# Kernel optimization log

Measured on AMD Instinct MI355X. Metric: run time of the kernel, lower is better.

Reference implementation:

```python
import jax, jax.numpy as jnp
import numpy as np

# GlobalAttention block from GATESynergy: to_dense_batch -> multi-head
# masked self-attention per graph -> scatter back to sparse + residual.
B, NMAX, DIN, DOUT, H = 512, 160, 128, 128, 4
DH = DOUT // H  # 32
COUNTS = np.where(np.arange(B) % 2 == 0, 96, 160)  # nodes per graph, sum=65536
T = int(COUNTS.sum())


def _xavier(key, dout, din):
    lim = np.sqrt(6.0 / (din + dout)).astype(np.float32)
    return jax.random.uniform(key, (dout, din), jnp.float32, -lim, lim)


def setup_inputs() -> dict:
    key = jax.random.key(0)
    ks = jax.random.split(key, 5)
    batch = jnp.asarray(np.repeat(np.arange(B), COUNTS), dtype=jnp.int32)
    x = jax.random.normal(ks[0], (T, DIN), jnp.float32)
    return {
        "x": x,
        "batch": batch,
        "Wq": _xavier(ks[1], DOUT, DIN), "bq": jnp.zeros((DOUT,), jnp.float32),
        "Wk": _xavier(ks[2], DOUT, DIN), "bk": jnp.zeros((DOUT,), jnp.float32),
        "Wv": _xavier(ks[3], DOUT, DIN), "bv": jnp.zeros((DOUT,), jnp.float32),
        "Wo": _xavier(ks[4], DOUT, DOUT), "bo": jnp.zeros((DOUT,), jnp.float32),
    }


def reference(x, batch, Wq, bq, Wk, bk, Wv, bv, Wo, bo):
    n = x.shape[0]
    # --- to_dense_batch: sparse [T, D] -> dense [B, NMAX, D] + mask ---
    counts = jax.ops.segment_sum(jnp.ones(n, jnp.int32), batch, num_segments=B)
    starts = jnp.cumsum(counts) - counts            # first node index per graph
    pos = jnp.arange(n, dtype=jnp.int32) - starts[batch]  # slot within graph
    x_dense = jnp.zeros((B, NMAX, DIN), x.dtype).at[batch, pos].set(x)
    mask = jnp.zeros((B, NMAX), bool).at[batch, pos].set(True)

    def proj(W, b):  # [B,N,DIN] -> [B,H,N,DH]
        return (x_dense @ W.T + b).reshape(B, NMAX, H, DH).transpose(0, 2, 1, 3)

    q, k, v = proj(Wq, bq), proj(Wk, bk), proj(Wv, bv)
    scores = jnp.einsum('bhnd,bhmd->bhnm', q, k) / jnp.sqrt(jnp.asarray(DH, x.dtype))
    scores = jnp.where(mask[:, None, None, :], scores, -jnp.inf)  # mask keys
    attn = jax.nn.softmax(scores, axis=-1)  # dropout p=0.0 -> identity
    out = jnp.einsum('bhnm,bhmd->bnhd', attn, v).reshape(B, NMAX, DOUT)
    out = out @ Wo.T + bo
    out_sparse = out[batch, pos]  # gather valid nodes back to sparse layout
    return out_sparse + x  # residual: in_channels == out_channels
```

## Files before the change

### kernel.cpp

```cpp
#include <hip/hip_runtime.h>

typedef unsigned short u16;
typedef unsigned int u32;
typedef __attribute__((ext_vector_type(8))) short bf16x8;
typedef __attribute__((ext_vector_type(4))) float f32x4;

__device__ __forceinline__ u16 f2bf(float f) {
  u32 u = __builtin_bit_cast(u32, f);
  u += 0x7fffu + ((u >> 16) & 1u);
  return (u16)(u >> 16);
}
__device__ __forceinline__ short f2bs(float f) { return (short)f2bf(f); }

__device__ __forceinline__ bf16x8 cvt8(const float* p) {
  f32x4 a = *reinterpret_cast<const f32x4*>(p);
  f32x4 b = *reinterpret_cast<const f32x4*>(p + 4);
  bf16x8 r;
  r[0] = f2bs(a[0]); r[1] = f2bs(a[1]); r[2] = f2bs(a[2]); r[3] = f2bs(a[3]);
  r[4] = f2bs(b[0]); r[5] = f2bs(b[1]); r[6] = f2bs(b[2]); r[7] = f2bs(b[3]);
  return r;
}
__device__ __forceinline__ bf16x8 lds8(const u16* p) {
  return *reinterpret_cast<const bf16x8*>(p);
}

#define MFMA(a, b, c) __builtin_amdgcn_mfma_f32_16x16x32_bf16((a), (b), (c), 0, 0, 0)

constexpr int DIN = 128, DOUT = 128, DH = 32;
constexpr int T = 65536;
constexpr size_t WFOFF = 0;
constexpr size_t QOFF = 65536;
constexpr size_t KOFF = QOFF + (size_t)4 * T * DH;
constexpr size_t VOFF = KOFF + (size_t)4 * T * DH;
constexpr size_t WS_NEED = (VOFF + (size_t)4 * T * DH) * 2;

__device__ __forceinline__ size_t fragoff(int mat, int ft, int ks) {
  return ((size_t)((mat * 8 + ft) * 4 + ks)) << 9;
}

__global__ void cvtw_kernel(const float* __restrict__ Wq, const float* __restrict__ Wk,
                            const float* __restrict__ Wv, const float* __restrict__ Wo,
                            u16* __restrict__ wf) {
  const int fl = blockIdx.x * 256 + threadIdx.x;
  const int lane = fl & 63, ks = (fl >> 6) & 3, ft = (fl >> 8) & 7, mat = fl >> 11;
  const float* src = mat == 0 ? Wq : mat == 1 ? Wk : mat == 2 ? Wv : Wo;
  const int lr = lane & 15, lg = lane >> 4;
  bf16x8 r = cvt8(src + (ft * 16 + lr) * DIN + ks * 32 + lg * 8);
  *reinterpret_cast<bf16x8*>(wf + (size_t)fl * 8) = r;
}

__global__ __launch_bounds__(256, 2) void qkv_kernel(const float* __restrict__ x,
                                                     const float* __restrict__ bq,
                                                     const float* __restrict__ bk,
                                                     const float* __restrict__ bv,
                                                     u16* __restrict__ ws) {
  const int tid = threadIdx.x;
  const int w = tid >> 6, lane = tid & 63, lg = lane >> 4, lr = lane & 15;
  const size_t rbase = (size_t)blockIdx.x * 128 + w * 32;
  const f32x4 zero = {0.f, 0.f, 0.f, 0.f};
  const u16* wf = ws + WFOFF;
  u16* Q = ws + QOFF;
  u16* K = ws + KOFF;
  u16* V = ws + VOFF;

  bf16x8 xa[2][4];
#pragma unroll
  for (int rt = 0; rt < 2; ++rt)
#pragma unroll
    for (int ks = 0; ks < 4; ++ks)
      xa[rt][ks] = cvt8(x + (rbase + rt * 16 + lr) * DIN + ks * 32 + lg * 8);

#pragma unroll
  for (int ft = 0; ft < 8; ++ft) {
    const int h = ft >> 1, dt = ft & 1;
    bf16x8 wqf[4], wkf[4], wvf[4];
#pragma unroll
    for (int ks = 0; ks < 4; ++ks) {
      wqf[ks] = lds8(wf + fragoff(0, ft, ks) + lane * 8);
      wkf[ks] = lds8(wf + fragoff(1, ft, ks) + lane * 8);
      wvf[ks] = lds8(wf + fragoff(2, ft, ks) + lane * 8);
    }
    f32x4 qacc[2], kacc[2], vacc[2];
#pragma unroll
    for (int rt = 0; rt < 2; ++rt) qacc[rt] = kacc[rt] = vacc[rt] = zero;
#pragma unroll
    for (int rt = 0; rt < 2; ++rt)
#pragma unroll
      for (int ks = 0; ks < 4; ++ks) {
        qacc[rt] = MFMA(xa[rt][ks], wqf[ks], qacc[rt]);
        kacc[rt] = MFMA(xa[rt][ks], wkf[ks], kacc[rt]);
        vacc[rt] = MFMA(wvf[ks], xa[rt][ks], vacc[rt]);
      }
    const float bqv = bq[ft * 16 + lr], bkv = bk[ft * 16 + lr];
    float bvj[4];
#pragma unroll
    for (int j = 0; j < 4; ++j) bvj[j] = bv[ft * 16 + lg * 4 + j];
#pragma unroll
    for (int rt = 0; rt < 2; ++rt) {
      const size_t row0 = rbase + rt * 16;
      const size_t qk_base = (size_t)h * T * DH + (row0 + lg * 4) * DH + dt * 16 + lr;
      const size_t v_base = (size_t)h * T * DH + (((rbase >> 5) + (rt >> 1)) << 10) +
                            (size_t)(dt * 16 + lg * 4) * 32 + (rt & 1) * 16 + lr;
#pragma unroll
      for (int j = 0; j < 4; ++j) {
        Q[qk_base + (size_t)j * DH] = f2bf(qacc[rt][j] + bqv);
        K[qk_base + (size_t)j * DH] = f2bf(kacc[rt][j] + bkv);
        V[v_base + (size_t)j * 32] = f2bf(vacc[rt][j] + bvj[j]);
      }
    }
  }
}

template <int C>
__device__ void attn_wave2(const u16* __restrict__ Qh, const u16* __restrict__ Kh,
                           const u16* __restrict__ Vh, const u16* __restrict__ wf,
                           const float* __restrict__ bo, const float* __restrict__ x,
                           float* __restrict__ out, int start, int h, int t0,
                           u16 (&strip)[16][168], u16 (&otile)[2][16][136]) {
  constexpr int NT = C / 16, KB = C / 32;
  const int lane = threadIdx.x & 63, lg = lane >> 4, lr = lane & 15;
  const f32x4 zero = {0.f, 0.f, 0.f, 0.f};
  const int w = h;

  bf16x8 vb[KB][2];
#pragma unroll
  for (int ks = 0; ks < KB; ++ks)
#pragma unroll
    for (int dt = 0; dt < 2; ++dt)
      vb[ks][dt] = lds8(Vh + (((size_t)(start >> 5) + ks) << 10) +
                        (size_t)(dt * 16 + lr) * 32 + lg * 8);
  bf16x8 kf[NT];
#pragma unroll
  for (int ct = 0; ct < NT; ++ct)
    kf[ct] = lds8(Kh + (size_t)(start + ct * 16 + lr) * DH + lg * 8);

#pragma unroll
  for (int r = 0; r < 2; ++r) {
    const int gr = start + (t0 + r) * 16;
    const bf16x8 qa = lds8(Qh + (size_t)(gr + lr) * DH + lg * 8);
    f32x4 sacc[NT];
#pragma unroll
    for (int ct = 0; ct < NT; ++ct) sacc[ct] = MFMA(qa, kf[ct], zero);

    const float scale = 0.17677669529663687f;
    float m[4], s[4];
#pragma unroll
    for (int j = 0; j < 4; ++j) {
      m[j] = sacc[0][j];
#pragma unroll
      for (int ct = 1; ct < NT; ++ct) m[j] = fmaxf(m[j], sacc[ct][j]);
    }
#pragma unroll
    for (int d = 1; d < 16; d <<= 1) {
#pragma unroll
      for (int j = 0; j < 4; ++j) m[j] = fmaxf(m[j], __shfl_xor(m[j], d, 64));
    }
#pragma unroll
    for (int j = 0; j < 4; ++j) {
      s[j] = 0.f;
#pragma unroll
      for (int ct = 0; ct < NT; ++ct) {
        const float p = __expf((sacc[ct][j] - m[j]) * scale);
        sacc[ct][j] = p;
        s[j] += p;
      }
    }
#pragma unroll
    for (int d = 1; d < 16; d <<= 1) {
#pragma unroll
      for (int j = 0; j < 4; ++j) s[j] += __shfl_xor(s[j], d, 64);
    }
#pragma unroll
    for (int j = 0; j < 4; ++j) {
      const float inv = 1.0f / s[j];
#pragma unroll
      for (int ct = 0; ct < NT; ++ct)
        strip[lg * 4 + j][ct * 16 + lr] = f2bf(sacc[ct][j] * inv);
    }
    asm volatile("s_waitcnt lgkmcnt(0)" ::: "memory");

    f32x4 o0 = zero, o1 = zero;
#pragma unroll
    for (int ks = 0; ks < KB; ++ks) {
      const bf16x8 pa = lds8(&strip[lr][ks * 32 + lg * 8]);
      o0 = MFMA(pa, vb[ks][0], o0);
      o1 = MFMA(pa, vb[ks][1], o1);
    }
#pragma unroll
    for (int j = 0; j < 4; ++j) {
      otile[r][lg * 4 + j][h * 32 + lr] = f2bf(o0[j]);
      otile[r][lg * 4 + j][h * 32 + 16 + lr] = f2bf(o1[j]);
    }
  }

  const int c0 = w * 32 + lr, c1 = w * 32 + 16 + lr;
  float xr0[2][4], xr1[2][4];
#pragma unroll
  for (int r = 0; r < 2; ++r) {
    const int gr = start + (t0 + r) * 16;
#pragma unroll
    for (int j = 0; j < 4; ++j) {
      const size_t n = (size_t)gr + lg * 4 + j;
      xr0[r][j] = x[n * DIN + c0];
      xr1[r][j] = x[n * DIN + c1];
    }
  }
  __syncthreads();

  const float b0 = bo[c0], b1 = bo[c1];
#pragma unroll
  for (int r = 0; r < 2; ++r) {
    bf16x8 oa[4];
#pragma unroll
    for (int ks = 0; ks < 4; ++ks) oa[ks] = lds8(&otile[r][lr][ks * 32 + lg * 8]);
    f32x4 acc0 = zero, acc1 = zero;
#pragma unroll
    for (int ks = 0; ks < 4; ++ks) {
      acc0 = MFMA(oa[ks], lds8(wf + fragoff(3, w * 2, ks) + lane * 8), acc0);
      acc1 = MFMA(oa[ks], lds8(wf + fragoff(3, w * 2 + 1, ks) + lane * 8), acc1);
    }
    const int gr = start + (t0 + r) * 16;
#pragma unroll
    for (int j = 0; j < 4; ++j) {
      const size_t n = (size_t)gr + lg * 4 + j;
      out[n * DOUT + c0] = acc0[j] + b0 + xr0[r][j];
      out[n * DOUT + c1] = acc1[j] + b1 + xr1[r][j];
    }
  }
}

__global__ __launch_bounds__(256, 3) void attn_kernel(const u16* __restrict__ ws,
                                                      const float* __restrict__ bo,
                                                      const float* __restrict__ x,
                                                      float* __restrict__ out) {
  __shared__ u16 strip[4][16][168];
  __shared__ u16 otile[2][16][136];
  const int w = threadIdx.x >> 6;
  const int phys = blockIdx.x;
  const int xcd = phys & 7, idx = phys >> 3;
  const int u = idx & 7;
  const int p = (idx >> 3) * 8 + xcd;
  const int h = w;
  const int t0 = u * 2;
  const u16* Qh = ws + QOFF + (size_t)h * T * DH;
  const u16* Kh = ws + KOFF + (size_t)h * T * DH;
  const u16* Vh = ws + VOFF + (size_t)h * T * DH;
  const u16* wf = ws + WFOFF;

  if (t0 < 6)
    attn_wave2<96>(Qh, Kh, Vh, wf, bo, x, out, p * 256, h, t0, strip[w], otile);
  else
    attn_wave2<160>(Qh, Kh, Vh, wf, bo, x, out, p * 256 + 96, h, t0 - 6, strip[w], otile);
}

struct SLds1 {
  u16 k[160][40];
  u16 vt[32][168];
  u16 strip[4][16][168];
};

template <int C>
__device__ void attn1(const float* __restrict__ xg, const float* __restrict__ Wq,
                      const float* __restrict__ bq, const float* __restrict__ Wk,
                      const float* __restrict__ bk, const float* __restrict__ Wv,
                      const float* __restrict__ bv, float* __restrict__ og, int h, SLds1& sm) {
  constexpr int NT = C / 16, KB = C / 32, SLOTS = (NT + 3) / 4;
  const int tid = threadIdx.x;
  const int w = tid >> 6, lane = tid & 63, lg = lane >> 4, lr = lane & 15;
  const f32x4 zero = {0.f, 0.f, 0.f, 0.f};

  for (int t = w; t < 2 * NT; t += 4) {
    const int rt = t >> 1, dt = t & 1;
    f32x4 kacc = zero, vacc = zero;
#pragma unroll
    for (int ks = 0; ks < 4; ++ks) {
      bf16x8 xa = cvt8(xg + (rt * 16 + lr) * DIN + ks * 32 + lg * 8);
      bf16x8 wk = cvt8(Wk + (h * DH + dt * 16 + lr) * DIN + ks * 32 + lg * 8);
      bf16x8 wv = cvt8(Wv + (h * DH + dt * 16 + lr) * DIN + ks * 32 + lg * 8);
      kacc = MFMA(xa, wk, kacc);
      vacc = MFMA(wv, xa, vacc);
    }
    const float kb_ = bk[h * DH + dt * 16 + lr];
#pragma unroll
    for (int j = 0; j < 4; ++j) {
      sm.k[rt * 16 + lg * 4 + j][dt * 16 + lr] = f2bf(kacc[j] + kb_);
      sm.vt[dt * 16 + lg * 4 + j][rt * 16 + lr] = f2bf(vacc[j] + bv[h * DH + dt * 16 + lg * 4 + j]);
    }
  }
  __syncthreads();

#pragma unroll
  for (int sl = 0; sl < SLOTS; ++sl) {
    const int rt = w + sl * 4;
    if (rt < NT) {
#pragma unroll
      for (int dt = 0; dt < 2; ++dt) {
        f32x4 qacc = zero;
#pragma unroll
        for (int ks = 0; ks < 4; ++ks) {
          bf16x8 xa = cvt8(xg + (rt * 16 + lr) * DIN + ks * 32 + lg * 8);
          bf16x8 wq = cvt8(Wq + (h * DH + dt * 16 + lr) * DIN + ks * 32 + lg * 8);
          qacc = MFMA(xa, wq, qacc);
        }
        const float bias = bq[h * DH + dt * 16 + lr];
#pragma unroll
        for (int j = 0; j < 4; ++j)
          sm.strip[w][lg * 4 + j][dt * 16 + lr] = f2bf(qacc[j] + bias);
      }
      asm volatile("s_waitcnt lgkmcnt(0)" ::: "memory");
      const bf16x8 qa = lds8(&sm.strip[w][lr][lg * 8]);
      f32x4 sacc[NT];
#pragma unroll
      for (int ct = 0; ct < NT; ++ct)
        sacc[ct] = MFMA(qa, lds8(&sm.k[ct * 16 + lr][lg * 8]), zero);
      const float scale = 0.17677669529663687f;
      float m[4], s[4];
#pragma unroll
      for (int j = 0; j < 4; ++j) {
        m[j] = sacc[0][j];
#pragma unroll
        for (int ct = 1; ct < NT; ++ct) m[j] = fmaxf(m[j], sacc[ct][j]);
      }
#pragma unroll
      for (int d = 1; d < 16; d <<= 1)
#pragma unroll
        for (int j = 0; j < 4; ++j) m[j] = fmaxf(m[j], __shfl_xor(m[j], d, 64));
#pragma unroll
      for (int j = 0; j < 4; ++j) {
        s[j] = 0.f;
#pragma unroll
        for (int ct = 0; ct < NT; ++ct) {
          const float p = __expf((sacc[ct][j] - m[j]) * scale);
          sacc[ct][j] = p;
          s[j] += p;
        }
      }
#pragma unroll
      for (int d = 1; d < 16; d <<= 1)
#pragma unroll
        for (int j = 0; j < 4; ++j) s[j] += __shfl_xor(s[j], d, 64);
#pragma unroll
      for (int j = 0; j < 4; ++j) {
        const float inv = 1.0f / s[j];
#pragma unroll
        for (int ct = 0; ct < NT; ++ct)
          sm.strip[w][lg * 4 + j][ct * 16 + lr] = f2bf(sacc[ct][j] * inv);
      }
      asm volatile("s_waitcnt lgkmcnt(0)" ::: "memory");
      f32x4 o0 = zero, o1 = zero;
#pragma unroll
      for (int ks = 0; ks < KB; ++ks) {
        const bf16x8 pa = lds8(&sm.strip[w][lr][ks * 32 + lg * 8]);
        o0 = MFMA(pa, lds8(&sm.vt[lr][ks * 32 + lg * 8]), o0);
        o1 = MFMA(pa, lds8(&sm.vt[16 + lr][ks * 32 + lg * 8]), o1);
      }
#pragma unroll
      for (int j = 0; j < 4; ++j) {
        const int n = rt * 16 + lg * 4 + j;
        og[n * DOUT + h * DH + lr] = o0[j];
        og[n * DOUT + h * DH + 16 + lr] = o1[j];
      }
    }
  }
}

__global__ __launch_bounds__(256, 3) void fb_k1(const float* __restrict__ x,
                                                const float* __restrict__ Wq,
                                                const float* __restrict__ bq,
                                                const float* __restrict__ Wk,
                                                const float* __restrict__ bk,
                                                const float* __restrict__ Wv,
                                                const float* __restrict__ bv,
                                                float* __restrict__ O) {
  __shared__ SLds1 sm;
  const int bid = blockIdx.x;
  const int g = bid >> 2, h = bid & 3;
  const int p = g >> 1;
  if (g & 1)
    attn1<160>(x + (size_t)(p * 256 + 96) * DIN, Wq, bq, Wk, bk, Wv, bv,
               O + (size_t)(p * 256 + 96) * DOUT, h, sm);
  else
    attn1<96>(x + (size_t)(p * 256) * DIN, Wq, bq, Wk, bk, Wv, bv, O + (size_t)(p * 256) * DOUT,
              h, sm);
}

__global__ __launch_bounds__(256, 4) void fb_k2(float* __restrict__ io, const float* __restrict__ x,
                                                const float* __restrict__ Wo,
                                                const float* __restrict__ bo) {
  const int tid = threadIdx.x;
  const int w = tid >> 6, lane = tid & 63, lg = lane >> 4, lr = lane & 15;
  const f32x4 zero = {0.f, 0.f, 0.f, 0.f};
  const int rbase = blockIdx.x * 128 + w * 32;
  bf16x8 oa[2][4];
#pragma unroll
  for (int r = 0; r < 2; ++r)
#pragma unroll
    for (int ks = 0; ks < 4; ++ks)
      oa[r][ks] = cvt8(io + (size_t)(rbase + r * 16 + lr) * DOUT + ks * 32 + lg * 8);
  f32x4 acc[2][8];
#pragma unroll
  for (int r = 0; r < 2; ++r)
#pragma unroll
    for (int jt = 0; jt < 8; ++jt) acc[r][jt] = zero;
#pragma unroll
  for (int jt = 0; jt < 8; ++jt)
#pragma unroll
    for (int ks = 0; ks < 4; ++ks) {
      const bf16x8 wb = cvt8(Wo + (size_t)(jt * 16 + lr) * DOUT + ks * 32 + lg * 8);
      acc[0][jt] = MFMA(oa[0][ks], wb, acc[0][jt]);
      acc[1][jt] = MFMA(oa[1][ks], wb, acc[1][jt]);
    }
#pragma unroll
  for (int r = 0; r < 2; ++r)
#pragma unroll
    for (int jt = 0; jt < 8; ++jt) {
      const int c = jt * 16 + lr;
      const float bias = bo[c];
#pragma unroll
      for (int j = 0; j < 4; ++j) {
        const size_t n = (size_t)rbase + r * 16 + lg * 4 + j;
        io[n * DOUT + c] = acc[r][jt][j] + bias + x[n * DIN + c];
      }
    }
}

extern "C" void kernel_launch(void* const* d_in, const int* in_sizes, int n_in,
                              void* d_out, int out_size, void* d_ws, size_t ws_size,
                              hipStream_t stream) {
  const float* x = (const float*)d_in[0];
  const float* Wq = (const float*)d_in[2];
  const float* bq = (const float*)d_in[3];
  const float* Wk = (const float*)d_in[4];
  const float* bk = (const float*)d_in[5];
  const float* Wv = (const float*)d_in[6];
  const float* bv = (const float*)d_in[7];
  const float* Wo = (const float*)d_in[8];
  const float* bo = (const float*)d_in[9];
  float* out = (float*)d_out;

  if (ws_size >= WS_NEED) {
    u16* ws = (u16*)d_ws;
    cvtw_kernel<<<dim3(32), dim3(256), 0, stream>>>(Wq, Wk, Wv, Wo, ws);
    qkv_kernel<<<dim3(512), dim3(256), 0, stream>>>(x, bq, bk, bv, ws);
    attn_kernel<<<dim3(2048), dim3(256), 0, stream>>>(ws, bo, x, out);
  } else {
    fb_k1<<<dim3(2048), dim3(256), 0, stream>>>(x, Wq, bq, Wk, bk, Wv, bv, out);
    fb_k2<<<dim3(512), dim3(256), 0, stream>>>(out, x, Wo, bo);
  }
}
```

Baseline: 57.52 us.

## Stage QKV outputs in LDS for vectorized stores and remap blocks across XCDs

```diff
diff --git a/kernel.cpp b/kernel.cpp
--- a/kernel.cpp
+++ b/kernel.cpp
@@ -54,9 +54,13 @@
                                                      const float* __restrict__ bk,
                                                      const float* __restrict__ bv,
                                                      u16* __restrict__ ws) {
+  __shared__ u16 tq[4][32][40], tk[4][32][40], tv[4][32][40];
   const int tid = threadIdx.x;
   const int w = tid >> 6, lane = tid & 63, lg = lane >> 4, lr = lane & 15;
-  const size_t rbase = (size_t)blockIdx.x * 128 + w * 32;
+  const int phys = blockIdx.x;
+  const int xcd = phys & 7, i = phys >> 3;
+  const int l = (((i >> 1) * 8 + xcd) << 1) | (i & 1);
+  const size_t rbase = (size_t)l * 128 + w * 32;
   const f32x4 zero = {0.f, 0.f, 0.f, 0.f};
   const u16* wf = ws + WFOFF;
   u16* Q = ws + QOFF;
@@ -71,42 +75,53 @@
       xa[rt][ks] = cvt8(x + (rbase + rt * 16 + lr) * DIN + ks * 32 + lg * 8);
 
 #pragma unroll
-  for (int ft = 0; ft < 8; ++ft) {
-    const int h = ft >> 1, dt = ft & 1;
-    bf16x8 wqf[4], wkf[4], wvf[4];
-#pragma unroll
-    for (int ks = 0; ks < 4; ++ks) {
-      wqf[ks] = lds8(wf + fragoff(0, ft, ks) + lane * 8);
-      wkf[ks] = lds8(wf + fragoff(1, ft, ks) + lane * 8);
-      wvf[ks] = lds8(wf + fragoff(2, ft, ks) + lane * 8);
-    }
-    f32x4 qacc[2], kacc[2], vacc[2];
-#pragma unroll
-    for (int rt = 0; rt < 2; ++rt) qacc[rt] = kacc[rt] = vacc[rt] = zero;
-#pragma unroll
-    for (int rt = 0; rt < 2; ++rt)
+  for (int h = 0; h < 4; ++h) {
+    f32x4 qacc[2][2], kacc[2][2], vacc[2][2];
+#pragma unroll
+    for (int dt = 0; dt < 2; ++dt) {
+      const int ft = h * 2 + dt;
+      bf16x8 wqf[4], wkf[4], wvf[4];
 #pragma unroll
       for (int ks = 0; ks < 4; ++ks) {
-        qacc[rt] = MFMA(xa[rt][ks], wqf[ks], qacc[rt]);
-        kacc[rt] = MFMA(xa[rt][ks], wkf[ks], kacc[rt]);
-        vacc[rt] = MFMA(wvf[ks], xa[rt][ks], vacc[rt]);
-      }
-    const float bqv = bq[ft * 16 + lr], bkv = bk[ft * 16 + lr];
-    float bvj[4];
-#pragma unroll
-    for (int j = 0; j < 4; ++j) bvj[j] = bv[ft * 16 + lg * 4 + j];
-#pragma unroll
-    for (int rt = 0; rt < 2; ++rt) {
-      const size_t row0 = rbase + rt * 16;
-      const size_t qk_base = (size_t)h * T * DH + (row0 + lg * 4) * DH + dt * 16 + lr;
-      const size_t v_base = (size_t)h * T * DH + (((rbase >> 5) + (rt >> 1)) << 10) +
-                            (size_t)(dt * 16 + lg * 4) * 32 + (rt & 1) * 16 + lr;
-#pragma unroll
-      for (int j = 0; j < 4; ++j) {
-        Q[qk_base + (size_t)j * DH] = f2bf(qacc[rt][j] + bqv);
-        K[qk_base + (size_t)j * DH] = f2bf(kacc[rt][j] + bkv);
-        V[v_base + (size_t)j * 32] = f2bf(vacc[rt][j] + bvj[j]);
-      }
+        wqf[ks] = lds8(wf + fragoff(0, ft, ks) + lane * 8);
+        wkf[ks] = lds8(wf + fragoff(1, ft, ks) + lane * 8);
+        wvf[ks] = lds8(wf + fragoff(2, ft, ks) + lane * 8);
+      }
+#pragma unroll
+      for (int rt = 0; rt < 2; ++rt) qacc[dt][rt] = kacc[dt][rt] = vacc[dt][rt] = zero;
+#pragma unroll
+      for (int rt = 0; rt < 2; ++rt)
+#pragma unroll
+        for (int ks = 0; ks < 4; ++ks) {
+          qacc[dt][rt] = MFMA(xa[rt][ks], wqf[ks], qacc[dt][rt]);
+          kacc[dt][rt] = MFMA(xa[rt][ks], wkf[ks], kacc[dt][rt]);
+          vacc[dt][rt] = MFMA(wvf[ks], xa[rt][ks], vacc[dt][rt]);
+        }
+    }
+#pragma unroll
+    for (int dt = 0; dt < 2; ++dt) {
+      const int ft = h * 2 + dt;
+      const float bqv = bq[ft * 16 + lr], bkv = bk[ft * 16 + lr];
+#pragma unroll
+      for (int rt = 0; rt < 2; ++rt)
+#pragma unroll
+        for (int j = 0; j < 4; ++j) {
+          tq[w][rt * 16 + lg * 4 + j][dt * 16 + lr] = f2bf(qacc[dt][rt][j] + bqv);
+          tk[w][rt * 16 + lg * 4 + j][dt * 16 + lr] = f2bf(kacc[dt][rt][j] + bkv);
+          tv[w][dt * 16 + lg * 4 + j][rt * 16 + lr] = f2bf(vacc[dt][rt][j] + bv[ft * 16 + lg * 4 + j]);
+        }
+    }
+    asm volatile("s_waitcnt lgkmcnt(0)" ::: "memory");
+    u16* Qb = Q + (size_t)h * T * DH + rbase * DH;
+    u16* Kb = K + (size_t)h * T * DH + rbase * DH;
+    u16* Vb = V + (size_t)h * T * DH + ((rbase >> 5) << 10);
+#pragma unroll
+    for (int s = 0; s < 2; ++s) {
+      const int g = lane * 16 + s * 8;
+      const int row = g >> 5, c = g & 31;
+      *reinterpret_cast<bf16x8*>(Qb + g) = lds8(&tq[w][row][c]);
+      *reinterpret_cast<bf16x8*>(Kb + g) = lds8(&tk[w][row][c]);
+      *reinterpret_cast<bf16x8*>(Vb + g) = lds8(&tv[w][row][c]);
     }
   }
 }
```

Result: slower. 66.27 us (+15.2%).
